# Kernel optimization log

Hardware: AMD Instinct MI355X
Metric: run time of the kernel (lower is better)

The kernel has to match this reference:

```python
import jax, jax.numpy as jnp
import numpy as np

# Binarize (sign) with straight-through estimator, matching the BNN-style
# BinarizeConv2d which replaces .data in-place (identity gradient path).
@jax.custom_vjp
def binarize(x):
    return jnp.where(x >= 0, 1.0, -1.0).astype(x.dtype)

def _bin_fwd(x):
    return binarize(x), None

def _bin_bwd(_, g):
    return (g,)

binarize.defvjp(_bin_fwd, _bin_bwd)

def conv2d(x, w, pad):
    # x: NCHW, w: OIHW, stride 1, symmetric 'same' padding for odd kernels
    return jax.lax.conv_general_dilated(
        x, w, window_strides=(1, 1), padding=[(pad, pad), (pad, pad)],
        dimension_numbers=("NCHW", "OIHW", "NCHW"))

def batchnorm2d(x, gamma, beta, eps=1e-5):
    # training-mode BatchNorm2d: batch statistics over (N, H, W)
    mean = jnp.mean(x, axis=(0, 2, 3), keepdims=True)
    var = jnp.var(x, axis=(0, 2, 3), keepdims=True)
    inv = gamma[None, :, None, None] * jax.lax.rsqrt(var + eps)
    return (x - mean) * inv + beta[None, :, None, None]

def leaky_relu(x, slope=0.5):
    return jnp.where(x >= 0, x, slope * x)

def setup_inputs() -> dict:
    key = jax.random.key(0)
    ks = jax.random.split(key, 4)
    B, H, W = 16, 256, 256
    x = jax.random.normal(ks[0], (B, 1, H, W), dtype=jnp.float32)
    w1 = jax.random.normal(ks[1], (128, 1, 7, 7), dtype=jnp.float32) * 0.1
    w2 = jax.random.normal(ks[2], (64, 128, 1, 1), dtype=jnp.float32) * 0.1
    w3 = jax.random.normal(ks[3], (1, 64, 5, 5), dtype=jnp.float32) * 0.05
    g1 = jnp.ones((128,), jnp.float32)
    b1 = jnp.zeros((128,), jnp.float32)
    g2 = jnp.ones((64,), jnp.float32)
    b2 = jnp.zeros((64,), jnp.float32)
    return {"x": x, "w1": w1, "g1": g1, "b1": b1,
            "w2": w2, "g2": g2, "b2": b2, "w3": w3}

def reference(x, w1, g1, b1, w2, g2, b2, w3):
    # layer1: binarized conv (in=1 channel != 3 -> input also binarized) + BN + LeakyReLU(0.5)
    h = conv2d(binarize(x), binarize(w1), pad=3)
    h = leaky_relu(batchnorm2d(h, g1, b1))
    # layer2: binarized 1x1 conv + BN + LeakyReLU(0.5)
    h = conv2d(binarize(h), binarize(w2), pad=0)
    h = leaky_relu(batchnorm2d(h, g2, b2))
    # layer3: plain full-precision 5x5 conv, no bias
    return conv2d(h, w3, pad=2)
```

## Files before the change

kernel.cpp:

```cpp
#include <hip/hip_runtime.h>
#include <cstdint>
#include <cstddef>
#include <climits>


#define NPIX_PER_CH (16.0 * 256.0 * 256.0)
#define PLANE_BYTES 67584
#define ROW_BYTES   264
#define FXSCALE     262144.0f
#define FXINV       3.814697265625e-06f

typedef _Float16 half2_t __attribute__((ext_vector_type(2)));

#if __has_builtin(__builtin_amdgcn_fdot2)
__device__ __forceinline__ float DOT2(half2_t a, half2_t b, float c) {
    return __builtin_amdgcn_fdot2(a, b, c, false);
}
#else
__device__ __forceinline__ float DOT2(half2_t a, half2_t b, float c) {
    return fmaf((float)a[0], (float)b[0], fmaf((float)a[1], (float)b[1], c));
}
#endif

__device__ __forceinline__ uint32_t pk_f16(float lo, float hi) {
#if __has_builtin(__builtin_amdgcn_cvt_pkrtz)
    auto h = __builtin_amdgcn_cvt_pkrtz(lo, hi);
    return __builtin_bit_cast(uint32_t, h);
#else
    half2_t h; h[0] = (_Float16)lo; h[1] = (_Float16)hi;
    return __builtin_bit_cast(uint32_t, h);
#endif
}
#define H2(u) __builtin_bit_cast(half2_t, (uint32_t)(u))

struct WS {
    int8_t*   h2s;
    uint64_t* xbits;
    uint64_t* wb1;
    uint64_t* w2lo;
    uint64_t* w2hi;
    uint4*    w2pk;
    long long* st1;
    long long* st2;
    uint4*    pk1;
    unsigned long long* flipm;
    float* a2; float* c2;
    uint32_t* wtab;
};

static inline WS carve(void* d_ws) {
    WS w;
    uint8_t* p = (uint8_t*)d_ws;
    w.h2s   = (int8_t*)p;              p += (size_t)16 * 64 * PLANE_BYTES;
    w.xbits = (uint64_t*)p;            p += (size_t)16 * 256 * 6 * 8;
    w.wb1   = (uint64_t*)p;            p += 128 * 8;
    w.w2lo  = (uint64_t*)p;            p += 64 * 8;
    w.w2hi  = (uint64_t*)p;            p += 64 * 8;
    w.w2pk  = (uint4*)p;               p += 64 * 16;
    w.st1   = (long long*)p;           p += 256 * 8;
    w.st2   = (long long*)p;           p += 128 * 8;
    w.pk1   = (uint4*)p;               p += 128 * 16;
    w.flipm = (unsigned long long*)p;  p += 2 * 8;
    w.a2    = (float*)p;               p += 64 * 4;
    w.c2    = (float*)p;               p += 64 * 4;
    w.wtab  = (uint32_t*)p;            p += 64 * 32 * 4;
    return w;
}

__global__ __launch_bounds__(256) void k_pack_x(const float* __restrict__ x,
                                                uint64_t* __restrict__ xbits) {
    int rowId = blockIdx.x * 4 + (threadIdx.x >> 6);
    int lane  = threadIdx.x & 63;
    const float* row = x + (size_t)rowId * 256;
    uint64_t b0 = __ballot(row[0 * 64 + lane] < 0.0f);
    uint64_t b1 = __ballot(row[1 * 64 + lane] < 0.0f);
    uint64_t b2 = __ballot(row[2 * 64 + lane] < 0.0f);
    uint64_t b3 = __ballot(row[3 * 64 + lane] < 0.0f);
    if (lane == 0) {
        uint64_t* o = xbits + (size_t)rowId * 6;
        o[0] = b0 << 8;
        o[1] = (b0 >> 56) | (b1 << 8);
        o[2] = (b1 >> 56) | (b2 << 8);
        o[3] = (b2 >> 56) | (b3 << 8);
        o[4] = b3 >> 56;
        o[5] = 0;
    }
}

__global__ void k_pack_w(const float* __restrict__ w1, const float* __restrict__ w2,
                         uint64_t* __restrict__ wb1, uint64_t* __restrict__ w2lo,
                         uint64_t* __restrict__ w2hi, uint4* __restrict__ w2pk,
                         long long* __restrict__ st1, long long* __restrict__ st2) {
    int t = threadIdx.x;
    if (t < 128) {
        uint64_t b = 0;
        for (int k = 0; k < 49; ++k)
            if (w1[t * 49 + k] < 0.0f) b |= (1ull << k);
        wb1[t] = b;
    } else if (t < 192) {
        int o = t - 128;
        uint64_t lo = 0, hi = 0;
        for (int c = 0; c < 64; ++c) if (w2[o * 128 + c]      < 0.0f) lo |= (1ull << c);
        for (int c = 0; c < 64; ++c) if (w2[o * 128 + 64 + c] < 0.0f) hi |= (1ull << c);
        w2lo[o] = lo; w2hi[o] = hi;
        w2pk[o] = make_uint4((uint32_t)lo, (uint32_t)(lo >> 32),
                             (uint32_t)hi, (uint32_t)(hi >> 32));
    }
    st1[t] = 0;
    if (t < 128) st2[t] = 0;
}

__device__ inline void build_window(const uint64_t* __restrict__ xb_img, int y, int x,
                                    uint64_t& sbits, uint64_t& vmask) {
    int bitpos = x + 5;
    int w  = bitpos >> 6;
    int sh = bitpos & 63;
    int lo = 3 - x;   if (lo < 0) lo = 0;
    int hi = 258 - x; if (hi > 6) hi = 6;
    uint64_t hm = ((1ull << (hi - lo + 1)) - 1ull) << lo;
    sbits = 0; vmask = 0;
    #pragma unroll
    for (int dy = 0; dy < 7; ++dy) {
        int yy = y - 3 + dy;
        if (yy < 0 || yy > 255) continue;
        const uint64_t* r = xb_img + (size_t)yy * 6;
        uint64_t wA = r[w], wB = r[w + 1];
        uint64_t bits = wA >> sh;
        if (sh) bits |= wB << (64 - sh);
        bits &= 0x7Full;
        sbits |= bits << (7 * dy);
        vmask |= hm   << (7 * dy);
    }
}

__global__ __launch_bounds__(256) void k_stats1(const uint64_t* __restrict__ xbits,
                                                const uint64_t* __restrict__ wb1g,
                                                long long* __restrict__ st1) {
    __shared__ uint64_t sb[256];
    __shared__ uint64_t vm[256];
    __shared__ int rs[128];
    __shared__ int rq[128];
    int t = threadIdx.x;
    int c = t & 127, half = t >> 7;
    uint64_t wb = wb1g[c];
    int sumE = 0, sqE = 0;
    int sumP = 0, sumPP = 0, nF = 0;
    for (int row = blockIdx.x; row < 4096; row += gridDim.x) {
        int n = row >> 8, y = row & 255;
        const uint64_t* xb_img = xbits + (size_t)n * 256 * 6;
        uint64_t s, v;
        build_window(xb_img, y, t, s, v);
        sb[t] = s; vm[t] = v;
        __syncthreads();
        int base = half << 7;
        auto edge = [&](int p) {
            uint64_t vv = vm[base + p];
            uint64_t d = (sb[base + p] ^ wb) & vv;
            int h = __popcll(vv) - 2 * __popcll(d);
            sumE += h; sqE += h * h;
        };
        if (y >= 3 && y <= 252) {
            int lo = (half == 0) ? 3 : 0;
            int hi = (half == 0) ? 128 : 125;
            for (int p = 0; p < lo; ++p) edge(p);
            #pragma unroll 4
            for (int p = lo; p < hi; ++p) {
                int pc = __popcll(sb[base + p] ^ wb);
                sumP += pc; sumPP += pc * pc;
            }
            for (int p = hi; p < 128; ++p) edge(p);
            nF += hi - lo;
        } else {
            #pragma unroll 4
            for (int p = 0; p < 128; ++p) edge(p);
        }
        __syncthreads();
    }
    int sum   = sumE + 49 * nF - 2 * sumP;
    int sumsq = sqE + 2401 * nF - 196 * sumP + 4 * sumPP;
    if (half == 1) { rs[c] = sum; rq[c] = sumsq; }
    __syncthreads();
    if (half == 0) {
        long long S = (long long)sum + rs[c];
        long long Q = (long long)sumsq + rq[c];
        atomicAdd((unsigned long long*)&st1[c],       (unsigned long long)S);
        atomicAdd((unsigned long long*)&st1[128 + c], (unsigned long long)Q);
    }
}

__global__ void k_fin1(const long long* __restrict__ st1,
                       const float* __restrict__ g1, const float* __restrict__ b1,
                       const uint64_t* __restrict__ wb1,
                       uint4* __restrict__ pk1, unsigned long long* __restrict__ flipm) {
    int c = threadIdx.x;
    double mean = (double)st1[c] / NPIX_PER_CH;
    double var  = (double)st1[128 + c] / NPIX_PER_CH - mean * mean;
    double a = (double)g1[c] / sqrt(var + 1e-5);
    double cst = (double)b1[c] - mean * a;
    int K; int flip = 0;
    if (a > 0.0) {
        double v = -cst / a;
        v = fmin(fmax(v, -100.0), 100.0);
        K = (int)ceil(v);
    } else if (a < 0.0) {
        double v = -cst / a;
        v = fmin(fmax(v, -100.0), 100.0);
        K = (int)floor(v) + 1; flip = 1;
    } else {
        K = INT_MIN; flip = (cst < 0.0) ? 1 : 0;
    }
    long long pt = ((49LL - (long long)K) >> 1) + 1;
    if (pt < 0) pt = 0;
    if (pt > 50) pt = 50;
    uint64_t wb = wb1[c];
    pk1[c] = make_uint4((uint32_t)wb, (uint32_t)(wb >> 32), (uint32_t)K, (uint32_t)pt);
    unsigned long long m = __ballot(flip != 0);
    if ((c & 63) == 0) flipm[c >> 6] = m;
}

__global__ __launch_bounds__(256) void k_conv2(const uint64_t* __restrict__ xbits,
                                               const uint4* __restrict__ pk1,
                                               const unsigned long long* __restrict__ flipm,
                                               const uint4* __restrict__ w2pk,
                                               int8_t* __restrict__ h2s) {
    int t = threadIdx.x;
    int n = blockIdx.x >> 8, y = blockIdx.x & 255, x = t;
    const uint64_t* xb_img = xbits + (size_t)n * 256 * 6;
    uint64_t sbits, vmask;
    build_window(xb_img, y, x, sbits, vmask);
    int nv = __popcll(vmask);

    uint32_t bw0 = 0, bw1 = 0, bw2 = 0, bw3 = 0;
    int wvid = __builtin_amdgcn_readfirstlane(t >> 6);
    bool fastw = (y >= 3 && y <= 252) && (wvid == 1 || wvid == 2);
    if (fastw) {
        #pragma unroll
        for (int cc = 0; cc < 128; ++cc) {
            uint4 pk = pk1[cc];
            uint64_t wb = ((uint64_t)pk.y << 32) | pk.x;
            int pc = __popcll(sbits ^ wb);
            uint32_t b = (uint32_t)(pc >= (int)pk.w) << (cc & 31);
            if (cc < 32)       bw0 |= b;
            else if (cc < 64)  bw1 |= b;
            else if (cc < 96)  bw2 |= b;
            else               bw3 |= b;
        }
    } else {
        #pragma unroll
        for (int cc = 0; cc < 128; ++cc) {
            uint4 pk = pk1[cc];
            uint64_t wb = ((uint64_t)pk.y << 32) | pk.x;
            int h = nv - 2 * __popcll((sbits ^ wb) & vmask);
            uint32_t b = (uint32_t)(h < (int)pk.z) << (cc & 31);
            if (cc < 32)       bw0 |= b;
            else if (cc < 64)  bw1 |= b;
            else if (cc < 96)  bw2 |= b;
            else               bw3 |= b;
        }
    }
    unsigned long long f0 = flipm[0], f1 = flipm[1];
    bw0 ^= (uint32_t)f0; bw1 ^= (uint32_t)(f0 >> 32);
    bw2 ^= (uint32_t)f1; bw3 ^= (uint32_t)(f1 >> 32);

    size_t base = (size_t)(n * 64) * PLANE_BYTES + (size_t)y * ROW_BYTES;
    #pragma unroll
    for (int o = 0; o < 64; ++o) {
        uint4 w = w2pk[o];
        int m = __popc(bw0 ^ w.x) + __popc(bw1 ^ w.y)
              + __popc(bw2 ^ w.z) + __popc(bw3 ^ w.w);
        h2s[base + (size_t)o * PLANE_BYTES + 2 + x] = (int8_t)(64 - m);
    }
    if (x == 0) {
        #pragma unroll 8
        for (int o = 0; o < 64; ++o)
            *(short*)(h2s + base + (size_t)o * PLANE_BYTES) = 0;
    }
    if (x == 255) {
        #pragma unroll 8
        for (int o = 0; o < 64; ++o) {
            int8_t* r = h2s + base + (size_t)o * PLANE_BYTES;
            *(short*)(r + 258) = 0;
            *(int*)(r + 260) = 0;
        }
    }
}

__global__ __launch_bounds__(256) void k_stats2(const int8_t* __restrict__ h2s,
                                                long long* __restrict__ st2) {
    int plane = blockIdx.x;
    int o = plane & 63;
    int t = threadIdx.x;
    const int4* p = (const int4*)(h2s + (size_t)plane * PLANE_BYTES);
    int sum = 0, sumsq = 0;
    for (int si = t; si < 4224; si += 256) {
        int4 v4 = p[si];
        int wv[4] = {v4.x, v4.y, v4.z, v4.w};
        #pragma unroll
        for (int j = 0; j < 4; ++j) {
            #pragma unroll
            for (int k = 0; k < 4; ++k) {
                int b = (int)(int8_t)((unsigned)wv[j] >> (8 * k));
                sum += b;
                sumsq += b * b;
            }
        }
    }
    for (int off = 32; off; off >>= 1) {
        sum   += __shfl_down(sum, off);
        sumsq += __shfl_down(sumsq, off);
    }
    __shared__ int ws1[4], ws2[4];
    int wid = t >> 6;
    if ((t & 63) == 0) { ws1[wid] = sum; ws2[wid] = sumsq; }
    __syncthreads();
    if (t == 0) {
        long long S = 0, Q = 0;
        for (int i = 0; i < 4; ++i) { S += ws1[i]; Q += ws2[i]; }
        atomicAdd((unsigned long long*)&st2[o],      (unsigned long long)S);
        atomicAdd((unsigned long long*)&st2[64 + o], (unsigned long long)Q);
    }
}

__global__ void k_fin2(const long long* __restrict__ st2,
                       const float* __restrict__ g2, const float* __restrict__ b2,
                       const float* __restrict__ w3,
                       float* __restrict__ a2, float* __restrict__ c2,
                       uint32_t* __restrict__ wtab) {
    int o = threadIdx.x;
    double mean = 2.0 * (double)st2[o] / NPIX_PER_CH;
    double msq  = 4.0 * (double)st2[64 + o] / NPIX_PER_CH;
    double var  = msq - mean * mean;
    double inv  = (double)g2[o] / sqrt(var + 1e-5);
    a2[o] = (float)(2.0 * inv);
    c2[o] = (float)((double)b2[o] - mean * inv);

    uint32_t* wp = wtab + o * 32;
    #pragma unroll
    for (int dy = 0; dy < 5; ++dy) {
        float w0 = w3[o * 25 + dy * 5 + 0];
        float w1 = w3[o * 25 + dy * 5 + 1];
        float w2v = w3[o * 25 + dy * 5 + 2];
        float w3v = w3[o * 25 + dy * 5 + 3];
        float w4 = w3[o * 25 + dy * 5 + 4];
        half2_t h;
        h[0] = (_Float16)w0;  h[1] = (_Float16)w1;  wp[dy*6+0] = __builtin_bit_cast(uint32_t, h);
        h[0] = (_Float16)w2v; h[1] = (_Float16)w3v; wp[dy*6+1] = __builtin_bit_cast(uint32_t, h);
        h[0] = (_Float16)w4;  h[1] = (_Float16)0.f; wp[dy*6+2] = __builtin_bit_cast(uint32_t, h);
        h[0] = (_Float16)0.f; h[1] = (_Float16)w0;  wp[dy*6+3] = __builtin_bit_cast(uint32_t, h);
        h[0] = (_Float16)w1;  h[1] = (_Float16)w2v; wp[dy*6+4] = __builtin_bit_cast(uint32_t, h);
        h[0] = (_Float16)w3v; h[1] = (_Float16)w4;  wp[dy*6+5] = __builtin_bit_cast(uint32_t, h);
    }
    wp[30] = 0; wp[31] = 0;
}

__global__ __launch_bounds__(256) void k_zero3(int4* __restrict__ o) {
    int i = blockIdx.x * 256 + threadIdx.x;
    #pragma unroll
    for (int j = 0; j < 4; ++j)
        o[(size_t)i * 4 + j] = make_int4(0, 0, 0, 0);
}

__global__ __launch_bounds__(256, 4) void k_conv3(const int8_t* __restrict__ h2s,
                                                  const float* __restrict__ a2g,
                                                  const float* __restrict__ c2g,
                                                  const uint32_t* __restrict__ wtab,
                                                  int* __restrict__ outi) {
    __shared__ uint16_t lds[4 * 36 * 72];
    __shared__ float sA2[16], sC2[16];
    int t = threadIdx.x;
    int bid = blockIdx.x;
    int cg   = bid >> 9;
    int rest = bid & 511;
    int n  = rest >> 5;
    int yt = (rest >> 2) & 7;
    int xt = rest & 3;
    int ty0 = yt * 32, tx0 = xt * 64;
    int cgbase = cg * 16;
    if (t < 16) { sA2[t] = a2g[cgbase + t]; sC2[t] = c2g[cgbase + t]; }

    int ty = t >> 4, tx = t & 15;
    int pbase = n * 64 + cgbase;

    int s_cl[10], s_lds[10];
    const int8_t* s_ptr[10];
    bool s_has[10], s_ok[10];
    #pragma unroll
    for (int it = 0; it < 10; ++it) {
        int si = t + 256 * it;
        int cl  = si / 612;
        int rem = si - cl * 612;
        int row = rem / 17;
        int q   = rem - row * 17;
        int gy  = ty0 - 2 + row;
        bool has = (si < 2448);
        bool ok  = has && ((unsigned)gy < 256u);
        s_cl[it]  = cl;
        s_lds[it] = cl * 2592 + row * 72 + q * 4;
        s_ptr[it] = h2s + (size_t)(pbase + (has ? cl : 0)) * PLANE_BYTES
                        + (size_t)(ok ? gy : 0) * ROW_BYTES + tx0 + q * 4;
        s_has[it] = has; s_ok[it] = ok;
    }
    int vv[10];
    #pragma unroll
    for (int it = 0; it < 10; ++it)
        vv[it] = s_ok[it] ? *(const int*)s_ptr[it] : 0;

    float acc[2][4] = {{0.f,0.f,0.f,0.f},{0.f,0.f,0.f,0.f}};

    for (int kk = 0; kk < 4; ++kk) {
        __syncthreads();
        #pragma unroll
        for (int it = 0; it < 10; ++it) {
            if (s_has[it]) {
                int lc = 4 * kk + s_cl[it];
                float a = sA2[lc], c = sC2[lc];
                int v = vv[it];
                float z0 = fmaf(a, (float)(int)(int8_t)(v),        c);
                float z1 = fmaf(a, (float)(int)(int8_t)(v >> 8),   c);
                float z2 = fmaf(a, (float)(int)(int8_t)(v >> 16),  c);
                float z3 = fmaf(a, (float)(int)(int8_t)(v >> 24),  c);
                z0 = fmaxf(z0, 0.5f * z0);
                z1 = fmaxf(z1, 0.5f * z1);
                z2 = fmaxf(z2, 0.5f * z2);
                z3 = fmaxf(z3, 0.5f * z3);
                uint2 wv2 = {pk_f16(z0, z1), pk_f16(z2, z3)};
                *(uint2*)(lds + s_lds[it]) = wv2;
            }
        }
        __syncthreads();
        if (kk < 3) {
            #pragma unroll
            for (int it = 0; it < 10; ++it) {
                s_ptr[it] += 4 * PLANE_BYTES;
                vv[it] = s_ok[it] ? *(const int*)s_ptr[it] : 0;
            }
        }

        #pragma unroll
        for (int cl = 0; cl < 4; ++cl) {
            const uint32_t* wp = wtab + (size_t)(cgbase + 4 * kk + cl) * 32;
            const uint16_t* base = lds + cl * 2592 + (2 * ty) * 72 + 4 * tx;
            uint2 A[6], B[6];
            #pragma unroll
            for (int rr = 0; rr < 6; ++rr) {
                A[rr] = *(const uint2*)(base + rr * 72);
                B[rr] = *(const uint2*)(base + rr * 72 + 4);
            }
            #pragma unroll
            for (int rr = 0; rr < 6; ++rr) {
                half2_t W0 = H2(A[rr].x), W1 = H2(A[rr].y);
                half2_t W2 = H2(B[rr].x), W3 = H2(B[rr].y);
                #pragma unroll
                for (int dyp = rr - 1; dyp <= rr; ++dyp) {
                    if (dyp < 0 || dyp > 4) continue;
                    int r = rr - dyp;
                    const uint32_t* wd = wp + dyp * 6;
                    acc[r][0] = DOT2(W0, H2(wd[0]), DOT2(W1, H2(wd[1]), DOT2(W2, H2(wd[2]), acc[r][0])));
                    acc[r][1] = DOT2(W0, H2(wd[3]), DOT2(W1, H2(wd[4]), DOT2(W2, H2(wd[5]), acc[r][1])));
                    acc[r][2] = DOT2(W1, H2(wd[0]), DOT2(W2, H2(wd[1]), DOT2(W3, H2(wd[2]), acc[r][2])));
                    acc[r][3] = DOT2(W1, H2(wd[3]), DOT2(W2, H2(wd[4]), DOT2(W3, H2(wd[5]), acc[r][3])));
                }
            }
        }
    }

    int ox = tx0 + 4 * tx;
    #pragma unroll
    for (int r = 0; r < 2; ++r) {
        int oy = ty0 + 2 * ty + r;
        size_t o = (size_t)n * 65536 + (size_t)oy * 256 + ox;
        #pragma unroll
        for (int j = 0; j < 4; ++j) {
            int q = __float2int_rn(acc[r][j] * FXSCALE);
            atomicAdd(outi + o + j, q);
        }
    }
}

__global__ __launch_bounds__(256) void k_fin3(int* __restrict__ o) {
    int i = blockIdx.x * 256 + threadIdx.x;
    int4 v = ((const int4*)o)[i];
    float4 f = {v.x * FXINV, v.y * FXINV, v.z * FXINV, v.w * FXINV};
    ((float4*)o)[i] = f;
}

extern "C" void kernel_launch(void* const* d_in, const int* in_sizes, int n_in,
                              void* d_out, int out_size, void* d_ws, size_t ws_size,
                              hipStream_t stream) {
    const float* x  = (const float*)d_in[0];
    const float* w1 = (const float*)d_in[1];
    const float* g1 = (const float*)d_in[2];
    const float* b1 = (const float*)d_in[3];
    const float* w2 = (const float*)d_in[4];
    const float* g2 = (const float*)d_in[5];
    const float* b2 = (const float*)d_in[6];
    const float* w3 = (const float*)d_in[7];

    WS ws = carve(d_ws);

    k_zero3<<<256, 256, 0, stream>>>((int4*)d_out);
    k_pack_x<<<1024, 256, 0, stream>>>(x, ws.xbits);
    k_pack_w<<<1, 256, 0, stream>>>(w1, w2, ws.wb1, ws.w2lo, ws.w2hi, ws.w2pk,
                                    ws.st1, ws.st2);
    k_stats1<<<2048, 256, 0, stream>>>(ws.xbits, ws.wb1, ws.st1);
    k_fin1<<<1, 128, 0, stream>>>(ws.st1, g1, b1, ws.wb1, ws.pk1, ws.flipm);
    k_conv2<<<4096, 256, 0, stream>>>(ws.xbits, ws.pk1, ws.flipm, ws.w2pk, ws.h2s);
    k_stats2<<<1024, 256, 0, stream>>>(ws.h2s, ws.st2);
    k_fin2<<<1, 64, 0, stream>>>(ws.st2, g2, b2, w3, ws.a2, ws.c2, ws.wtab);
    k_conv3<<<2048, 256, 0, stream>>>(ws.h2s, ws.a2, ws.c2, ws.wtab, (int*)d_out);
    k_fin3<<<1024, 256, 0, stream>>>((int*)d_out);
}
```

Baseline: 223.6 us.

## Drop channel-split atomics in conv3; each block reduces all 64 channels

The final 5x5 conv no longer splits the 64 input channels across four block groups with fixed-point integer atomicAdd. Each 512-thread block now loops over all 64 channels in 8 chunks of 8 and writes float4 results directly, which removes the zero-fill and int-to-float finalize kernels. Each thread now computes one output row instead of two, so vertical window reuse across rows is lost, LDS use doubles, and the grid shrinks to 512 blocks, which may underfill the GPU.

Result: faster. 209.8 us (-6.2%).

```diff
diff --git a/kernel.cpp b/kernel.cpp
--- a/kernel.cpp
+++ b/kernel.cpp
@@ -7,8 +7,6 @@
 #define NPIX_PER_CH (16.0 * 256.0 * 256.0)
 #define PLANE_BYTES 67584
 #define ROW_BYTES   264
-#define FXSCALE     262144.0f
-#define FXINV       3.814697265625e-06f
 
 typedef _Float16 half2_t __attribute__((ext_vector_type(2)));
 
@@ -353,46 +351,36 @@
     wp[30] = 0; wp[31] = 0;
 }
 
-__global__ __launch_bounds__(256) void k_zero3(int4* __restrict__ o) {
-    int i = blockIdx.x * 256 + threadIdx.x;
-    #pragma unroll
-    for (int j = 0; j < 4; ++j)
-        o[(size_t)i * 4 + j] = make_int4(0, 0, 0, 0);
-}
-
-__global__ __launch_bounds__(256, 4) void k_conv3(const int8_t* __restrict__ h2s,
+__global__ __launch_bounds__(512, 4) void k_conv3(const int8_t* __restrict__ h2s,
                                                   const float* __restrict__ a2g,
                                                   const float* __restrict__ c2g,
                                                   const uint32_t* __restrict__ wtab,
-                                                  int* __restrict__ outi) {
-    __shared__ uint16_t lds[4 * 36 * 72];
-    __shared__ float sA2[16], sC2[16];
+                                                  float* __restrict__ out) {
+    __shared__ uint16_t lds[8 * 36 * 72];
+    __shared__ float sA2[64], sC2[64];
     int t = threadIdx.x;
     int bid = blockIdx.x;
-    int cg   = bid >> 9;
-    int rest = bid & 511;
-    int n  = rest >> 5;
-    int yt = (rest >> 2) & 7;
-    int xt = rest & 3;
+    int n  = bid >> 5;
+    int yt = (bid >> 2) & 7;
+    int xt = bid & 3;
     int ty0 = yt * 32, tx0 = xt * 64;
-    int cgbase = cg * 16;
-    if (t < 16) { sA2[t] = a2g[cgbase + t]; sC2[t] = c2g[cgbase + t]; }
+    if (t < 64) { sA2[t] = a2g[t]; sC2[t] = c2g[t]; }
 
     int ty = t >> 4, tx = t & 15;
-    int pbase = n * 64 + cgbase;
+    int pbase = n * 64;
 
     int s_cl[10], s_lds[10];
     const int8_t* s_ptr[10];
     bool s_has[10], s_ok[10];
     #pragma unroll
     for (int it = 0; it < 10; ++it) {
-        int si = t + 256 * it;
+        int si = t + 512 * it;
         int cl  = si / 612;
         int rem = si - cl * 612;
         int row = rem / 17;
         int q   = rem - row * 17;
         int gy  = ty0 - 2 + row;
-        bool has = (si < 2448);
+        bool has = (si < 4896);
         bool ok  = has && ((unsigned)gy < 256u);
         s_cl[it]  = cl;
         s_lds[it] = cl * 2592 + row * 72 + q * 4;
@@ -405,14 +393,14 @@
     for (int it = 0; it < 10; ++it)
         vv[it] = s_ok[it] ? *(const int*)s_ptr[it] : 0;
 
-    float acc[2][4] = {{0.f,0.f,0.f,0.f},{0.f,0.f,0.f,0.f}};
-
-    for (int kk = 0; kk < 4; ++kk) {
+    float acc[4] = {0.f, 0.f, 0.f, 0.f};
+
+    for (int kk = 0; kk < 8; ++kk) {
         __syncthreads();
         #pragma unroll
         for (int it = 0; it < 10; ++it) {
             if (s_has[it]) {
-                int lc = 4 * kk + s_cl[it];
+                int lc = 8 * kk + s_cl[it];
                 float a = sA2[lc], c = sC2[lc];
                 int v = vv[it];
                 float z0 = fmaf(a, (float)(int)(int8_t)(v),        c);
@@ -428,60 +416,41 @@
             }
         }
         __syncthreads();
-        if (kk < 3) {
+        if (kk < 7) {
             #pragma unroll
             for (int it = 0; it < 10; ++it) {
-                s_ptr[it] += 4 * PLANE_BYTES;
+                s_ptr[it] += 8 * PLANE_BYTES;
                 vv[it] = s_ok[it] ? *(const int*)s_ptr[it] : 0;
             }
         }
 
         #pragma unroll
-        for (int cl = 0; cl < 4; ++cl) {
-            const uint32_t* wp = wtab + (size_t)(cgbase + 4 * kk + cl) * 32;
-            const uint16_t* base = lds + cl * 2592 + (2 * ty) * 72 + 4 * tx;
-            uint2 A[6], B[6];
+        for (int cl = 0; cl < 8; ++cl) {
+            const uint32_t* wp = wtab + (size_t)(8 * kk + cl) * 32;
+            const uint16_t* base = lds + cl * 2592 + ty * 72 + 4 * tx;
+            uint2 A[5], B[5];
             #pragma unroll
-            for (int rr = 0; rr < 6; ++rr) {
+            for (int rr = 0; rr < 5; ++rr) {
                 A[rr] = *(const uint2*)(base + rr * 72);
                 B[rr] = *(const uint2*)(base + rr * 72 + 4);
             }
             #pragma unroll
-            for (int rr = 0; rr < 6; ++rr) {
+            for (int rr = 0; rr < 5; ++rr) {
                 half2_t W0 = H2(A[rr].x), W1 = H2(A[rr].y);
                 half2_t W2 = H2(B[rr].x), W3 = H2(B[rr].y);
-                #pragma unroll
-                for (int dyp = rr - 1; dyp <= rr; ++dyp) {
-                    if (dyp < 0 || dyp > 4) continue;
-                    int r = rr - dyp;
-                    const uint32_t* wd = wp + dyp * 6;
-                    acc[r][0] = DOT2(W0, H2(wd[0]), DOT2(W1, H2(wd[1]), DOT2(W2, H2(wd[2]), acc[r][0])));
-                    acc[r][1] = DOT2(W0, H2(wd[3]), DOT2(W1, H2(wd[4]), DOT2(W2, H2(wd[5]), acc[r][1])));
-                    acc[r][2] = DOT2(W1, H2(wd[0]), DOT2(W2, H2(wd[1]), DOT2(W3, H2(wd[2]), acc[r][2])));
-                    acc[r][3] = DOT2(W1, H2(wd[3]), DOT2(W2, H2(wd[4]), DOT2(W3, H2(wd[5]), acc[r][3])));
-                }
-            }
-        }
-    }
-
+                const uint32_t* wd = wp + rr * 6;
+                acc[0] = DOT2(W0, H2(wd[0]), DOT2(W1, H2(wd[1]), DOT2(W2, H2(wd[2]), acc[0])));
+                acc[1] = DOT2(W0, H2(wd[3]), DOT2(W1, H2(wd[4]), DOT2(W2, H2(wd[5]), acc[1])));
+                acc[2] = DOT2(W1, H2(wd[0]), DOT2(W2, H2(wd[1]), DOT2(W3, H2(wd[2]), acc[2])));
+                acc[3] = DOT2(W1, H2(wd[3]), DOT2(W2, H2(wd[4]), DOT2(W3, H2(wd[5]), acc[3])));
+            }
+        }
+    }
+
+    int oy = ty0 + ty;
     int ox = tx0 + 4 * tx;
-    #pragma unroll
-    for (int r = 0; r < 2; ++r) {
-        int oy = ty0 + 2 * ty + r;
-        size_t o = (size_t)n * 65536 + (size_t)oy * 256 + ox;
-        #pragma unroll
-        for (int j = 0; j < 4; ++j) {
-            int q = __float2int_rn(acc[r][j] * FXSCALE);
-            atomicAdd(outi + o + j, q);
-        }
-    }
-}
-
-__global__ __launch_bounds__(256) void k_fin3(int* __restrict__ o) {
-    int i = blockIdx.x * 256 + threadIdx.x;
-    int4 v = ((const int4*)o)[i];
-    float4 f = {v.x * FXINV, v.y * FXINV, v.z * FXINV, v.w * FXINV};
-    ((float4*)o)[i] = f;
+    float4 r = {acc[0], acc[1], acc[2], acc[3]};
+    *(float4*)(out + (size_t)n * 65536 + (size_t)oy * 256 + ox) = r;
 }
 
 extern "C" void kernel_launch(void* const* d_in, const int* in_sizes, int n_in,
@@ -495,10 +464,10 @@
     const float* g2 = (const float*)d_in[5];
     const float* b2 = (const float*)d_in[6];
     const float* w3 = (const float*)d_in[7];
+    float* out = (float*)d_out;
 
     WS ws = carve(d_ws);
 
-    k_zero3<<<256, 256, 0, stream>>>((int4*)d_out);
     k_pack_x<<<1024, 256, 0, stream>>>(x, ws.xbits);
     k_pack_w<<<1, 256, 0, stream>>>(w1, w2, ws.wb1, ws.w2lo, ws.w2hi, ws.w2pk,
                                     ws.st1, ws.st2);
@@ -507,6 +476,5 @@
     k_conv2<<<4096, 256, 0, stream>>>(ws.xbits, ws.pk1, ws.flipm, ws.w2pk, ws.h2s);
     k_stats2<<<1024, 256, 0, stream>>>(ws.h2s, ws.st2);
     k_fin2<<<1, 64, 0, stream>>>(ws.st2, g2, b2, w3, ws.a2, ws.c2, ws.wtab);
-    k_conv3<<<2048, 256, 0, stream>>>(ws.h2s, ws.a2, ws.c2, ws.wtab, (int*)d_out);
-    k_fin3<<<1024, 256, 0, stream>>>((int*)d_out);
-}
+    k_conv3<<<512, 512, 0, stream>>>(ws.h2s, ws.a2, ws.c2, ws.wtab, out);
+}
```

## Drop channel split in conv3, accumulate all 64 channels per block

Applied to the files above, without the earlier changes.

The final 5x5 conv previously split the 64 input channels across 4 channel groups, and each group atomically added fixed-point partial sums into a zeroed output. A separate kernel then converted the sums to float. Now each block loops over all 64 channels and writes its float4 results directly. This removes the zero and finalize kernels and the integer atomics, but cuts the grid from 2048 to 512 blocks, which lowers parallelism on a large GPU.

After: 225.8 us. About the same (+0.9%).

```diff
diff --git a/kernel.cpp b/kernel.cpp
--- a/kernel.cpp
+++ b/kernel.cpp
@@ -7,8 +7,6 @@
 #define NPIX_PER_CH (16.0 * 256.0 * 256.0)
 #define PLANE_BYTES 67584
 #define ROW_BYTES   264
-#define FXSCALE     262144.0f
-#define FXINV       3.814697265625e-06f
 
 typedef _Float16 half2_t __attribute__((ext_vector_type(2)));
 
@@ -353,33 +351,23 @@
     wp[30] = 0; wp[31] = 0;
 }
 
-__global__ __launch_bounds__(256) void k_zero3(int4* __restrict__ o) {
-    int i = blockIdx.x * 256 + threadIdx.x;
-    #pragma unroll
-    for (int j = 0; j < 4; ++j)
-        o[(size_t)i * 4 + j] = make_int4(0, 0, 0, 0);
-}
-
 __global__ __launch_bounds__(256, 4) void k_conv3(const int8_t* __restrict__ h2s,
                                                   const float* __restrict__ a2g,
                                                   const float* __restrict__ c2g,
                                                   const uint32_t* __restrict__ wtab,
-                                                  int* __restrict__ outi) {
+                                                  float* __restrict__ out) {
     __shared__ uint16_t lds[4 * 36 * 72];
-    __shared__ float sA2[16], sC2[16];
+    __shared__ float sA2[64], sC2[64];
     int t = threadIdx.x;
     int bid = blockIdx.x;
-    int cg   = bid >> 9;
-    int rest = bid & 511;
-    int n  = rest >> 5;
-    int yt = (rest >> 2) & 7;
-    int xt = rest & 3;
+    int n  = bid >> 5;
+    int yt = (bid >> 2) & 7;
+    int xt = bid & 3;
     int ty0 = yt * 32, tx0 = xt * 64;
-    int cgbase = cg * 16;
-    if (t < 16) { sA2[t] = a2g[cgbase + t]; sC2[t] = c2g[cgbase + t]; }
+    if (t < 64) { sA2[t] = a2g[t]; sC2[t] = c2g[t]; }
 
     int ty = t >> 4, tx = t & 15;
-    int pbase = n * 64 + cgbase;
+    int pbase = n * 64;
 
     int s_cl[10], s_lds[10];
     const int8_t* s_ptr[10];
@@ -394,9 +382,10 @@
         int gy  = ty0 - 2 + row;
         bool has = (si < 2448);
         bool ok  = has && ((unsigned)gy < 256u);
-        s_cl[it]  = cl;
-        s_lds[it] = cl * 2592 + row * 72 + q * 4;
-        s_ptr[it] = h2s + (size_t)(pbase + (has ? cl : 0)) * PLANE_BYTES
+        int clc = has ? cl : 0;
+        s_cl[it]  = clc;
+        s_lds[it] = clc * 2592 + row * 72 + q * 4;
+        s_ptr[it] = h2s + (size_t)(pbase + clc) * PLANE_BYTES
                         + (size_t)(ok ? gy : 0) * ROW_BYTES + tx0 + q * 4;
         s_has[it] = has; s_ok[it] = ok;
     }
@@ -407,7 +396,7 @@
 
     float acc[2][4] = {{0.f,0.f,0.f,0.f},{0.f,0.f,0.f,0.f}};
 
-    for (int kk = 0; kk < 4; ++kk) {
+    for (int kk = 0; kk < 16; ++kk) {
         __syncthreads();
         #pragma unroll
         for (int it = 0; it < 10; ++it) {
@@ -428,7 +417,7 @@
             }
         }
         __syncthreads();
-        if (kk < 3) {
+        if (kk < 15) {
             #pragma unroll
             for (int it = 0; it < 10; ++it) {
                 s_ptr[it] += 4 * PLANE_BYTES;
@@ -438,7 +427,7 @@
 
         #pragma unroll
         for (int cl = 0; cl < 4; ++cl) {
-            const uint32_t* wp = wtab + (size_t)(cgbase + 4 * kk + cl) * 32;
+            const uint32_t* wp = wtab + (size_t)(4 * kk + cl) * 32;
             const uint16_t* base = lds + cl * 2592 + (2 * ty) * 72 + 4 * tx;
             uint2 A[6], B[6];
             #pragma unroll
@@ -468,20 +457,9 @@
     #pragma unroll
     for (int r = 0; r < 2; ++r) {
         int oy = ty0 + 2 * ty + r;
-        size_t o = (size_t)n * 65536 + (size_t)oy * 256 + ox;
-        #pragma unroll
-        for (int j = 0; j < 4; ++j) {
-            int q = __float2int_rn(acc[r][j] * FXSCALE);
-            atomicAdd(outi + o + j, q);
-        }
-    }
-}
-
-__global__ __launch_bounds__(256) void k_fin3(int* __restrict__ o) {
-    int i = blockIdx.x * 256 + threadIdx.x;
-    int4 v = ((const int4*)o)[i];
-    float4 f = {v.x * FXINV, v.y * FXINV, v.z * FXINV, v.w * FXINV};
-    ((float4*)o)[i] = f;
+        float4 rv = {acc[r][0], acc[r][1], acc[r][2], acc[r][3]};
+        *(float4*)(out + (size_t)n * 65536 + (size_t)oy * 256 + ox) = rv;
+    }
 }
 
 extern "C" void kernel_launch(void* const* d_in, const int* in_sizes, int n_in,
@@ -495,10 +473,10 @@
     const float* g2 = (const float*)d_in[5];
     const float* b2 = (const float*)d_in[6];
     const float* w3 = (const float*)d_in[7];
+    float* out = (float*)d_out;
 
     WS ws = carve(d_ws);
 
-    k_zero3<<<256, 256, 0, stream>>>((int4*)d_out);
     k_pack_x<<<1024, 256, 0, stream>>>(x, ws.xbits);
     k_pack_w<<<1, 256, 0, stream>>>(w1, w2, ws.wb1, ws.w2lo, ws.w2hi, ws.w2pk,
                                     ws.st1, ws.st2);
@@ -507,6 +485,5 @@
     k_conv2<<<4096, 256, 0, stream>>>(ws.xbits, ws.pk1, ws.flipm, ws.w2pk, ws.h2s);
     k_stats2<<<1024, 256, 0, stream>>>(ws.h2s, ws.st2);
     k_fin2<<<1, 64, 0, stream>>>(ws.st2, g2, b2, w3, ws.a2, ws.c2, ws.wtab);
-    k_conv3<<<2048, 256, 0, stream>>>(ws.h2s, ws.a2, ws.c2, ws.wtab, (int*)d_out);
-    k_fin3<<<1024, 256, 0, stream>>>((int*)d_out);
-}
+    k_conv3<<<512, 256, 0, stream>>>(ws.h2s, ws.a2, ws.c2, ws.wtab, out);
+}
```
